# Performance work log

Hardware: AMD Instinct MI355X
Metric: run time of the kernel (lower is better)

Reference implementation:

```python
import jax, jax.numpy as jnp
import numpy as np

N, M, G, D = 64, 8, 64, 4
TAU_SPECIES = 5.0

def _psd(key, batch_shape):
    # random SPD matrices: 0.3*A A^T + 0.5 I
    A = 0.3 * jax.random.normal(key, (*batch_shape, D, D), dtype=jnp.float32)
    I = jnp.eye(D, dtype=jnp.float32)
    return jnp.einsum('...ij,...kj->...ik', A, A) + 0.5 * I

def _invertible(key, batch_shape):
    I = jnp.eye(D, dtype=jnp.float32)
    return I + 0.1 * jax.random.normal(key, (*batch_shape, D, D), dtype=jnp.float32)

def setup_inputs() -> dict:
    key = jax.random.key(0)
    ks = jax.random.split(key, 7)
    return {
        'mu_a': jax.random.normal(ks[0], (N, G, G, D), dtype=jnp.float32),
        'sigma_a': _psd(ks[1], (N, G, G)),
        'omega_a': _invertible(ks[2], (N, G, G)),
        'mu_b': jax.random.normal(ks[3], (M, G, G, D), dtype=jnp.float32),
        'sigma_b': _psd(ks[4], (M, G, G)),
        'omega_b': _invertible(ks[5], (M, G, G)),
        'chi': jax.random.uniform(ks[6], (N, G, G), dtype=jnp.float32),
    }

def reference(mu_a, sigma_a, omega_a, mu_b, sigma_b, omega_b, chi):
    # transport: Omega_a @ Omega_b^{-1}, pairwise over (N, M) and pointwise over grid
    omega_b_inv = jnp.linalg.inv(omega_b)                                  # (M,G,G,D,D)
    transport = jnp.einsum('nghij,mghjk->nmghik', omega_a, omega_b_inv)    # (N,M,G,G,D,D)
    mu_b_t = jnp.einsum('nmghij,mghj->nmghi', transport, mu_b)             # (N,M,G,G,D)
    sigma_b_t = jnp.einsum('nmghij,mghjk,nmghlk->nmghil',
                           transport, sigma_b, transport)                  # (N,M,G,G,D,D)
    # KL( N(mu_a, sigma_a) || N(mu_b_t, sigma_b_t) ), pointwise
    sig_b_inv = jnp.linalg.inv(sigma_b_t)
    diff = mu_a[:, None] - mu_b_t                                          # (N,M,G,G,D)
    tr = jnp.einsum('nmghij,nghji->nmgh', sig_b_inv, sigma_a)
    mahal = jnp.einsum('nmghi,nmghij,nmghj->nmgh', diff, sig_b_inv, diff)
    ld_b = jnp.linalg.slogdet(sigma_b_t)[1]                                # (N,M,G,G)
    ld_a = jnp.linalg.slogdet(sigma_a)[1]                                  # (N,G,G)
    kl = 0.5 * (tr + mahal - D + ld_b - ld_a[:, None])
    # species gate, masked by agent support chi_i(x)
    S = jax.nn.sigmoid(-kl / TAU_SPECIES) * chi[:, None]
    return S
```

## Files before the change

### kernel.cpp

```cpp
#include <hip/hip_runtime.h>
#include <math.h>


namespace {

constexpr int kN = 64;
constexpr int kM = 8;
constexpr int kG = 64;
constexpr int kGH = kG * kG;
constexpr int kMB = kM * kGH;
constexpr float kInvTau = 1.0f / 5.0f;

__device__ __forceinline__ void load16(const float* __restrict__ p, int idx,
                                       float* __restrict__ o) {
    const float4* p4 = reinterpret_cast<const float4*>(p);
#pragma unroll
    for (int k = 0; k < 4; ++k) {
        float4 v = p4[idx * 4 + k];
        o[4 * k + 0] = v.x;
        o[4 * k + 1] = v.y;
        o[4 * k + 2] = v.z;
        o[4 * k + 3] = v.w;
    }
}

__device__ __forceinline__ float det4(const float* __restrict__ m) {
    float s0 = m[0] * m[5] - m[1] * m[4];
    float s1 = m[0] * m[6] - m[2] * m[4];
    float s2 = m[0] * m[7] - m[3] * m[4];
    float s3 = m[1] * m[6] - m[2] * m[5];
    float s4 = m[1] * m[7] - m[3] * m[5];
    float s5 = m[2] * m[7] - m[3] * m[6];
    float c5 = m[10] * m[15] - m[11] * m[14];
    float c4 = m[9] * m[15] - m[11] * m[13];
    float c3 = m[9] * m[14] - m[10] * m[13];
    float c2 = m[8] * m[15] - m[11] * m[12];
    float c1 = m[8] * m[14] - m[10] * m[12];
    float c0 = m[8] * m[13] - m[9] * m[12];
    return s0 * c5 - s1 * c4 + s2 * c3 + s3 * c2 - s4 * c1 + s5 * c0;
}

__device__ __forceinline__ float inv4(const float* __restrict__ m,
                                      float* __restrict__ inv) {
    float s0 = m[0] * m[5] - m[1] * m[4];
    float s1 = m[0] * m[6] - m[2] * m[4];
    float s2 = m[0] * m[7] - m[3] * m[4];
    float s3 = m[1] * m[6] - m[2] * m[5];
    float s4 = m[1] * m[7] - m[3] * m[5];
    float s5 = m[2] * m[7] - m[3] * m[6];
    float c5 = m[10] * m[15] - m[11] * m[14];
    float c4 = m[9] * m[15] - m[11] * m[13];
    float c3 = m[9] * m[14] - m[10] * m[13];
    float c2 = m[8] * m[15] - m[11] * m[12];
    float c1 = m[8] * m[14] - m[10] * m[12];
    float c0 = m[8] * m[13] - m[9] * m[12];
    float det = s0 * c5 - s1 * c4 + s2 * c3 + s3 * c2 - s4 * c1 + s5 * c0;
    float r = __builtin_amdgcn_rcpf(det);
    inv[0]  = ( m[5]  * c5 - m[6]  * c4 + m[7]  * c3) * r;
    inv[1]  = (-m[1]  * c5 + m[2]  * c4 - m[3]  * c3) * r;
    inv[2]  = ( m[13] * s5 - m[14] * s4 + m[15] * s3) * r;
    inv[3]  = (-m[9]  * s5 + m[10] * s4 - m[11] * s3) * r;
    inv[4]  = (-m[4]  * c5 + m[6]  * c2 - m[7]  * c1) * r;
    inv[5]  = ( m[0]  * c5 - m[2]  * c2 + m[3]  * c1) * r;
    inv[6]  = (-m[12] * s5 + m[14] * s2 - m[15] * s1) * r;
    inv[7]  = ( m[8]  * s5 - m[10] * s2 + m[11] * s1) * r;
    inv[8]  = ( m[4]  * c4 - m[5]  * c2 + m[7]  * c0) * r;
    inv[9]  = (-m[0]  * c4 + m[1]  * c2 - m[3]  * c0) * r;
    inv[10] = ( m[12] * s4 - m[13] * s2 + m[15] * s0) * r;
    inv[11] = (-m[8]  * s4 + m[9]  * s2 - m[11] * s0) * r;
    inv[12] = (-m[4]  * c3 + m[5]  * c1 - m[6]  * c0) * r;
    inv[13] = ( m[0]  * c3 - m[1]  * c1 + m[2]  * c0) * r;
    inv[14] = (-m[12] * s3 + m[13] * s1 - m[14] * s0) * r;
    inv[15] = ( m[8]  * s3 - m[9]  * s1 + m[10] * s0) * r;
    return det;
}

__global__ __launch_bounds__(256) void precompute_b_kernel(
    const float* __restrict__ mu_b,
    const float* __restrict__ sigma_b,
    const float* __restrict__ omega_b,
    float4* __restrict__ ws)
{
    const int idx = blockIdx.x * blockDim.x + threadIdx.x;
    float Sb[16], Ob[16];
    load16(sigma_b, idx, Sb);
    load16(omega_b, idx, Ob);
    float SbI[16], ObI[16];
    const float detSb = inv4(Sb, SbI);
    const float detOb = inv4(Ob, ObI);
    const float4 mb4 = reinterpret_cast<const float4*>(mu_b)[idx];
    const float mb[4] = {mb4.x, mb4.y, mb4.z, mb4.w};

    float R[16];
#pragma unroll
    for (int i = 0; i < 4; ++i)
#pragma unroll
        for (int k = 0; k < 4; ++k)
            R[i * 4 + k] = SbI[i * 4 + 0] * Ob[0 * 4 + k]
                         + SbI[i * 4 + 1] * Ob[1 * 4 + k]
                         + SbI[i * 4 + 2] * Ob[2 * 4 + k]
                         + SbI[i * 4 + 3] * Ob[3 * 4 + k];
    float Qf[10];
    int pi = 0;
#pragma unroll
    for (int i = 0; i < 4; ++i)
#pragma unroll
        for (int k = 0; k < 4; ++k) {
            if (k < i) continue;
            float q = Ob[0 * 4 + i] * R[0 * 4 + k]
                    + Ob[1 * 4 + i] * R[1 * 4 + k]
                    + Ob[2 * 4 + i] * R[2 * 4 + k]
                    + Ob[3 * 4 + i] * R[3 * 4 + k];
            Qf[pi++] = (i == k) ? q : 2.0f * q;
        }
    float v[4];
#pragma unroll
    for (int i = 0; i < 4; ++i)
        v[i] = ObI[i * 4 + 0] * mb[0] + ObI[i * 4 + 1] * mb[1]
             + ObI[i * 4 + 2] * mb[2] + ObI[i * 4 + 3] * mb[3];

    const float lb = __logf(fabsf(detSb)) - 2.0f * __logf(fabsf(detOb));

    ws[0 * kMB + idx] = make_float4(Qf[0], Qf[1], Qf[2], Qf[3]);
    ws[1 * kMB + idx] = make_float4(Qf[4], Qf[5], Qf[6], Qf[7]);
    ws[2 * kMB + idx] = make_float4(Qf[8], Qf[9], lb, 0.0f);
    ws[3 * kMB + idx] = make_float4(v[0], v[1], v[2], v[3]);
}

__global__ __launch_bounds__(256) void species_kernel(
    const float* __restrict__ mu_a,
    const float* __restrict__ sigma_a,
    const float* __restrict__ omega_a,
    const float* __restrict__ chi,
    const float4* __restrict__ ws,
    float* __restrict__ out)
{
    const int t = blockIdx.x * blockDim.x + threadIdx.x;
    const int gh = t & (kGH - 1);
    const int n = t >> 12;

    float Sa[16], Oa[16], OaI[16];
    load16(sigma_a, t, Sa);
    load16(omega_a, t, Oa);
    const float detOa = inv4(Oa, OaI);
    const float detSa = det4(Sa);
    const float la = __logf(fabsf(detSa)) - 2.0f * __logf(fabsf(detOa));
    const float4 ma4 = reinterpret_cast<const float4*>(mu_a)[t];
    const float ma[4] = {ma4.x, ma4.y, ma4.z, ma4.w};
    const float x = chi[t];

    float w[4];
#pragma unroll
    for (int i = 0; i < 4; ++i)
        w[i] = OaI[i * 4 + 0] * ma[0] + OaI[i * 4 + 1] * ma[1]
             + OaI[i * 4 + 2] * ma[2] + OaI[i * 4 + 3] * ma[3];

    float Mt[16];
#pragma unroll
    for (int i = 0; i < 4; ++i)
#pragma unroll
        for (int k = 0; k < 4; ++k)
            Mt[i * 4 + k] = OaI[i * 4 + 0] * Sa[0 * 4 + k]
                          + OaI[i * 4 + 1] * Sa[1 * 4 + k]
                          + OaI[i * 4 + 2] * Sa[2 * 4 + k]
                          + OaI[i * 4 + 3] * Sa[3 * 4 + k];
    float Pf[10];
    {
        int pi = 0;
#pragma unroll
        for (int i = 0; i < 4; ++i)
#pragma unroll
            for (int k = 0; k < 4; ++k) {
                if (k < i) continue;
                Pf[pi++] = Mt[i * 4 + 0] * OaI[k * 4 + 0]
                         + Mt[i * 4 + 1] * OaI[k * 4 + 1]
                         + Mt[i * 4 + 2] * OaI[k * 4 + 2]
                         + Mt[i * 4 + 3] * OaI[k * 4 + 3];
            }
    }

#pragma unroll
    for (int m = 0; m < kM; ++m) {
        const int bb = m * kGH + gh;
        const float4 q0 = ws[0 * kMB + bb];
        const float4 q1 = ws[1 * kMB + bb];
        const float4 q2 = ws[2 * kMB + bb];
        const float4 q3 = ws[3 * kMB + bb];

        const float u0 = w[0] - q3.x;
        const float u1 = w[1] - q3.y;
        const float u2 = w[2] - q3.z;
        const float u3 = w[3] - q3.w;

        float tr = q0.x * Pf[0] + q0.y * Pf[1] + q0.z * Pf[2] + q0.w * Pf[3]
                 + q1.x * Pf[4] + q1.y * Pf[5] + q1.z * Pf[6] + q1.w * Pf[7]
                 + q2.x * Pf[8] + q2.y * Pf[9];
        float mah = q0.x * (u0 * u0) + q0.y * (u0 * u1) + q0.z * (u0 * u2)
                  + q0.w * (u0 * u3) + q1.x * (u1 * u1) + q1.y * (u1 * u2)
                  + q1.z * (u1 * u3) + q1.w * (u2 * u2) + q2.x * (u2 * u3)
                  + q2.y * (u3 * u3);

        const float kl = 0.5f * (tr + mah - 4.0f + q2.z - la);
        const float e = __expf(kl * kInvTau);
        const float s = x * __builtin_amdgcn_rcpf(1.0f + e);
        out[(n * kM + m) * kGH + gh] = s;
    }
}

}

extern "C" void kernel_launch(void* const* d_in, const int* in_sizes, int n_in,
                              void* d_out, int out_size, void* d_ws, size_t ws_size,
                              hipStream_t stream) {
    const float* mu_a    = (const float*)d_in[0];
    const float* sigma_a = (const float*)d_in[1];
    const float* omega_a = (const float*)d_in[2];
    const float* mu_b    = (const float*)d_in[3];
    const float* sigma_b = (const float*)d_in[4];
    const float* omega_b = (const float*)d_in[5];
    const float* chi     = (const float*)d_in[6];
    float* out = (float*)d_out;
    float4* ws = (float4*)d_ws;

    precompute_b_kernel<<<kMB / 256, 256, 0, stream>>>(mu_b, sigma_b, omega_b, ws);

    const int threads = kN * kGH;
    species_kernel<<<threads / 256, 256, 0, stream>>>(
        mu_a, sigma_a, omega_a, chi, ws, out);
}
```

Baseline: 98.22 us.

## Split species kernel across M with shared-memory staged coalesced A loads

Each block now handles 64 grid points, with four thread rows each computing two of the eight M outputs instead of one thread computing all eight. The sigma_a and omega_a matrices are loaded cooperatively with coalesced float4 reads into padded shared memory and then read back per thread. This raises thread-level parallelism and fixes the strided per-thread global loads. In exchange, every row redundantly recomputes the per-point A-side inverse and quadratic forms, adding a barrier and four times the A-side arithmetic.

```diff
diff --git a/kernel.cpp b/kernel.cpp
--- a/kernel.cpp
+++ b/kernel.cpp
@@ -10,6 +10,7 @@
 constexpr int kGH = kG * kG;
 constexpr int kMB = kM * kGH;
 constexpr float kInvTau = 1.0f / 5.0f;
+constexpr int kPad = 20;
 
 __device__ __forceinline__ void load16(const float* __restrict__ p, int idx,
                                        float* __restrict__ o) {
@@ -135,19 +136,41 @@
     const float4* __restrict__ ws,
     float* __restrict__ out)
 {
-    const int t = blockIdx.x * blockDim.x + threadIdx.x;
-    const int gh = t & (kGH - 1);
-    const int n = t >> 12;
+    __shared__ float sS[64 * kPad];
+    __shared__ float sO[64 * kPad];
+
+    const int x = threadIdx.x;
+    const int y = threadIdx.y;
+    const int tid = y * 64 + x;
+    const int t0 = blockIdx.x * 64;
+    const int t = t0 + x;
+    const int gh = (t0 & (kGH - 1)) + x;
+    const int n = t0 >> 12;
+
+    {
+        const float4* gs = reinterpret_cast<const float4*>(sigma_a) + (size_t)t0 * 4;
+        const float4* go = reinterpret_cast<const float4*>(omega_a) + (size_t)t0 * 4;
+        const float4 vs = gs[tid];
+        const float4 vo = go[tid];
+        const int xr = tid >> 2;
+        const int kk = (tid & 3) * 4;
+        *reinterpret_cast<float4*>(&sS[xr * kPad + kk]) = vs;
+        *reinterpret_cast<float4*>(&sO[xr * kPad + kk]) = vo;
+    }
+    __syncthreads();
 
     float Sa[16], Oa[16], OaI[16];
-    load16(sigma_a, t, Sa);
-    load16(omega_a, t, Oa);
+#pragma unroll
+    for (int j = 0; j < 16; ++j) {
+        Sa[j] = sS[x * kPad + j];
+        Oa[j] = sO[x * kPad + j];
+    }
     const float detOa = inv4(Oa, OaI);
     const float detSa = det4(Sa);
     const float la = __logf(fabsf(detSa)) - 2.0f * __logf(fabsf(detOa));
     const float4 ma4 = reinterpret_cast<const float4*>(mu_a)[t];
     const float ma[4] = {ma4.x, ma4.y, ma4.z, ma4.w};
-    const float x = chi[t];
+    const float xchi = chi[t];
 
     float w[4];
 #pragma unroll
@@ -180,7 +203,8 @@
     }
 
 #pragma unroll
-    for (int m = 0; m < kM; ++m) {
+    for (int h = 0; h < 2; ++h) {
+        const int m = y + 4 * h;
         const int bb = m * kGH + gh;
         const float4 q0 = ws[0 * kMB + bb];
         const float4 q1 = ws[1 * kMB + bb];
@@ -202,7 +226,7 @@
 
         const float kl = 0.5f * (tr + mah - 4.0f + q2.z - la);
         const float e = __expf(kl * kInvTau);
-        const float s = x * __builtin_amdgcn_rcpf(1.0f + e);
+        const float s = xchi * __builtin_amdgcn_rcpf(1.0f + e);
         out[(n * kM + m) * kGH + gh] = s;
     }
 }
@@ -224,7 +248,7 @@
 
     precompute_b_kernel<<<kMB / 256, 256, 0, stream>>>(mu_b, sigma_b, omega_b, ws);
 
-    const int threads = kN * kGH;
-    species_kernel<<<threads / 256, 256, 0, stream>>>(
+    dim3 block(64, 4);
+    species_kernel<<<kN * kGH / 64, block, 0, stream>>>(
         mu_a, sigma_a, omega_a, chi, ws, out);
 }
```

After: 99.67 us. About the same (+1.5%).

## Move per-A precompute into merged precompute kernel alongside B precompute

Applied to the files above, without the earlier changes.

Merges the B-side and A-side per-point precomputation into one kernel launch using block-index dispatch, writing A-side quadratic form terms, log-determinant, chi and transformed mean to workspace. The species kernel then only reads precomputed A and B factors and evaluates the pairwise KL gate. This aims to fill the GPU during the small B precompute and slim the main kernel, at the cost of extra workspace write and read traffic for the A terms.

```diff
diff --git a/kernel.cpp b/kernel.cpp
--- a/kernel.cpp
+++ b/kernel.cpp
@@ -9,6 +9,7 @@
 constexpr int kG = 64;
 constexpr int kGH = kG * kG;
 constexpr int kMB = kM * kGH;
+constexpr int kNA = kN * kGH;
 constexpr float kInvTau = 1.0f / 5.0f;
 
 __device__ __forceinline__ void load16(const float* __restrict__ p, int idx,
@@ -75,97 +76,90 @@
     return det;
 }
 
-__global__ __launch_bounds__(256) void precompute_b_kernel(
+__global__ __launch_bounds__(256) void precompute_kernel(
+    const float* __restrict__ mu_a,
+    const float* __restrict__ sigma_a,
+    const float* __restrict__ omega_a,
+    const float* __restrict__ chi,
     const float* __restrict__ mu_b,
     const float* __restrict__ sigma_b,
     const float* __restrict__ omega_b,
     float4* __restrict__ ws)
 {
-    const int idx = blockIdx.x * blockDim.x + threadIdx.x;
-    float Sb[16], Ob[16];
-    load16(sigma_b, idx, Sb);
-    load16(omega_b, idx, Ob);
-    float SbI[16], ObI[16];
-    const float detSb = inv4(Sb, SbI);
-    const float detOb = inv4(Ob, ObI);
-    const float4 mb4 = reinterpret_cast<const float4*>(mu_b)[idx];
-    const float mb[4] = {mb4.x, mb4.y, mb4.z, mb4.w};
-
-    float R[16];
-#pragma unroll
-    for (int i = 0; i < 4; ++i)
-#pragma unroll
-        for (int k = 0; k < 4; ++k)
-            R[i * 4 + k] = SbI[i * 4 + 0] * Ob[0 * 4 + k]
-                         + SbI[i * 4 + 1] * Ob[1 * 4 + k]
-                         + SbI[i * 4 + 2] * Ob[2 * 4 + k]
-                         + SbI[i * 4 + 3] * Ob[3 * 4 + k];
-    float Qf[10];
-    int pi = 0;
-#pragma unroll
-    for (int i = 0; i < 4; ++i)
-#pragma unroll
-        for (int k = 0; k < 4; ++k) {
-            if (k < i) continue;
-            float q = Ob[0 * 4 + i] * R[0 * 4 + k]
-                    + Ob[1 * 4 + i] * R[1 * 4 + k]
-                    + Ob[2 * 4 + i] * R[2 * 4 + k]
-                    + Ob[3 * 4 + i] * R[3 * 4 + k];
-            Qf[pi++] = (i == k) ? q : 2.0f * q;
-        }
-    float v[4];
-#pragma unroll
-    for (int i = 0; i < 4; ++i)
-        v[i] = ObI[i * 4 + 0] * mb[0] + ObI[i * 4 + 1] * mb[1]
-             + ObI[i * 4 + 2] * mb[2] + ObI[i * 4 + 3] * mb[3];
-
-    const float lb = __logf(fabsf(detSb)) - 2.0f * __logf(fabsf(detOb));
-
-    ws[0 * kMB + idx] = make_float4(Qf[0], Qf[1], Qf[2], Qf[3]);
-    ws[1 * kMB + idx] = make_float4(Qf[4], Qf[5], Qf[6], Qf[7]);
-    ws[2 * kMB + idx] = make_float4(Qf[8], Qf[9], lb, 0.0f);
-    ws[3 * kMB + idx] = make_float4(v[0], v[1], v[2], v[3]);
-}
-
-__global__ __launch_bounds__(256) void species_kernel(
-    const float* __restrict__ mu_a,
-    const float* __restrict__ sigma_a,
-    const float* __restrict__ omega_a,
-    const float* __restrict__ chi,
-    const float4* __restrict__ ws,
-    float* __restrict__ out)
-{
-    const int t = blockIdx.x * blockDim.x + threadIdx.x;
-    const int gh = t & (kGH - 1);
-    const int n = t >> 12;
-
-    float Sa[16], Oa[16], OaI[16];
-    load16(sigma_a, t, Sa);
-    load16(omega_a, t, Oa);
-    const float detOa = inv4(Oa, OaI);
-    const float detSa = det4(Sa);
-    const float la = __logf(fabsf(detSa)) - 2.0f * __logf(fabsf(detOa));
-    const float4 ma4 = reinterpret_cast<const float4*>(mu_a)[t];
-    const float ma[4] = {ma4.x, ma4.y, ma4.z, ma4.w};
-    const float x = chi[t];
-
-    float w[4];
-#pragma unroll
-    for (int i = 0; i < 4; ++i)
-        w[i] = OaI[i * 4 + 0] * ma[0] + OaI[i * 4 + 1] * ma[1]
-             + OaI[i * 4 + 2] * ma[2] + OaI[i * 4 + 3] * ma[3];
-
-    float Mt[16];
-#pragma unroll
-    for (int i = 0; i < 4; ++i)
-#pragma unroll
-        for (int k = 0; k < 4; ++k)
-            Mt[i * 4 + k] = OaI[i * 4 + 0] * Sa[0 * 4 + k]
-                          + OaI[i * 4 + 1] * Sa[1 * 4 + k]
-                          + OaI[i * 4 + 2] * Sa[2 * 4 + k]
-                          + OaI[i * 4 + 3] * Sa[3 * 4 + k];
-    float Pf[10];
-    {
+    const int blk = blockIdx.x;
+    if (blk < kMB / 256) {
+        const int idx = blk * 256 + threadIdx.x;
+        float Sb[16], Ob[16];
+        load16(sigma_b, idx, Sb);
+        load16(omega_b, idx, Ob);
+        float SbI[16], ObI[16];
+        const float detSb = inv4(Sb, SbI);
+        const float detOb = inv4(Ob, ObI);
+        const float4 mb4 = reinterpret_cast<const float4*>(mu_b)[idx];
+        const float mb[4] = {mb4.x, mb4.y, mb4.z, mb4.w};
+
+        float R[16];
+#pragma unroll
+        for (int i = 0; i < 4; ++i)
+#pragma unroll
+            for (int k = 0; k < 4; ++k)
+                R[i * 4 + k] = SbI[i * 4 + 0] * Ob[0 * 4 + k]
+                             + SbI[i * 4 + 1] * Ob[1 * 4 + k]
+                             + SbI[i * 4 + 2] * Ob[2 * 4 + k]
+                             + SbI[i * 4 + 3] * Ob[3 * 4 + k];
+        float Qf[10];
+        int pi = 0;
+#pragma unroll
+        for (int i = 0; i < 4; ++i)
+#pragma unroll
+            for (int k = 0; k < 4; ++k) {
+                if (k < i) continue;
+                float q = Ob[0 * 4 + i] * R[0 * 4 + k]
+                        + Ob[1 * 4 + i] * R[1 * 4 + k]
+                        + Ob[2 * 4 + i] * R[2 * 4 + k]
+                        + Ob[3 * 4 + i] * R[3 * 4 + k];
+                Qf[pi++] = (i == k) ? q : 2.0f * q;
+            }
+        float v[4];
+#pragma unroll
+        for (int i = 0; i < 4; ++i)
+            v[i] = ObI[i * 4 + 0] * mb[0] + ObI[i * 4 + 1] * mb[1]
+                 + ObI[i * 4 + 2] * mb[2] + ObI[i * 4 + 3] * mb[3];
+
+        const float lb = __logf(fabsf(detSb)) - 2.0f * __logf(fabsf(detOb));
+
+        ws[0 * kMB + idx] = make_float4(Qf[0], Qf[1], Qf[2], Qf[3]);
+        ws[1 * kMB + idx] = make_float4(Qf[4], Qf[5], Qf[6], Qf[7]);
+        ws[2 * kMB + idx] = make_float4(Qf[8], Qf[9], lb, 0.0f);
+        ws[3 * kMB + idx] = make_float4(v[0], v[1], v[2], v[3]);
+    } else {
+        const int t = (blk - kMB / 256) * 256 + threadIdx.x;
+        float Sa[16], Oa[16], OaI[16];
+        load16(sigma_a, t, Sa);
+        load16(omega_a, t, Oa);
+        const float detOa = inv4(Oa, OaI);
+        const float detSa = det4(Sa);
+        const float la = __logf(fabsf(detSa)) - 2.0f * __logf(fabsf(detOa));
+        const float4 ma4 = reinterpret_cast<const float4*>(mu_a)[t];
+        const float ma[4] = {ma4.x, ma4.y, ma4.z, ma4.w};
+        const float xchi = chi[t];
+
+        float w[4];
+#pragma unroll
+        for (int i = 0; i < 4; ++i)
+            w[i] = OaI[i * 4 + 0] * ma[0] + OaI[i * 4 + 1] * ma[1]
+                 + OaI[i * 4 + 2] * ma[2] + OaI[i * 4 + 3] * ma[3];
+
+        float Mt[16];
+#pragma unroll
+        for (int i = 0; i < 4; ++i)
+#pragma unroll
+            for (int k = 0; k < 4; ++k)
+                Mt[i * 4 + k] = OaI[i * 4 + 0] * Sa[0 * 4 + k]
+                              + OaI[i * 4 + 1] * Sa[1 * 4 + k]
+                              + OaI[i * 4 + 2] * Sa[2 * 4 + k]
+                              + OaI[i * 4 + 3] * Sa[3 * 4 + k];
+        float Pf[10];
         int pi = 0;
 #pragma unroll
         for (int i = 0; i < 4; ++i)
@@ -177,7 +171,30 @@
                          + Mt[i * 4 + 2] * OaI[k * 4 + 2]
                          + Mt[i * 4 + 3] * OaI[k * 4 + 3];
             }
+
+        float4* wsA = ws + 4 * kMB;
+        wsA[0 * kNA + t] = make_float4(Pf[0], Pf[1], Pf[2], Pf[3]);
+        wsA[1 * kNA + t] = make_float4(Pf[4], Pf[5], Pf[6], Pf[7]);
+        wsA[2 * kNA + t] = make_float4(Pf[8], Pf[9], la, xchi);
+        wsA[3 * kNA + t] = make_float4(w[0], w[1], w[2], w[3]);
     }
+}
+
+__global__ __launch_bounds__(256) void species_kernel(
+    const float4* __restrict__ ws,
+    float* __restrict__ out)
+{
+    const int t = blockIdx.x * blockDim.x + threadIdx.x;
+    const int gh = t & (kGH - 1);
+    const int n = t >> 12;
+
+    const float4* __restrict__ wsA = ws + 4 * kMB;
+    const float4 a0 = wsA[0 * kNA + t];
+    const float4 a1 = wsA[1 * kNA + t];
+    const float4 a2 = wsA[2 * kNA + t];
+    const float4 a3 = wsA[3 * kNA + t];
+    const float la = a2.z;
+    const float xchi = a2.w;
 
 #pragma unroll
     for (int m = 0; m < kM; ++m) {
@@ -187,14 +204,14 @@
         const float4 q2 = ws[2 * kMB + bb];
         const float4 q3 = ws[3 * kMB + bb];
 
-        const float u0 = w[0] - q3.x;
-        const float u1 = w[1] - q3.y;
-        const float u2 = w[2] - q3.z;
-        const float u3 = w[3] - q3.w;
-
-        float tr = q0.x * Pf[0] + q0.y * Pf[1] + q0.z * Pf[2] + q0.w * Pf[3]
-                 + q1.x * Pf[4] + q1.y * Pf[5] + q1.z * Pf[6] + q1.w * Pf[7]
-                 + q2.x * Pf[8] + q2.y * Pf[9];
+        const float u0 = a3.x - q3.x;
+        const float u1 = a3.y - q3.y;
+        const float u2 = a3.z - q3.z;
+        const float u3 = a3.w - q3.w;
+
+        float tr = q0.x * a0.x + q0.y * a0.y + q0.z * a0.z + q0.w * a0.w
+                 + q1.x * a1.x + q1.y * a1.y + q1.z * a1.z + q1.w * a1.w
+                 + q2.x * a2.x + q2.y * a2.y;
         float mah = q0.x * (u0 * u0) + q0.y * (u0 * u1) + q0.z * (u0 * u2)
                   + q0.w * (u0 * u3) + q1.x * (u1 * u1) + q1.y * (u1 * u2)
                   + q1.z * (u1 * u3) + q1.w * (u2 * u2) + q2.x * (u2 * u3)
@@ -202,7 +219,7 @@
 
         const float kl = 0.5f * (tr + mah - 4.0f + q2.z - la);
         const float e = __expf(kl * kInvTau);
-        const float s = x * __builtin_amdgcn_rcpf(1.0f + e);
+        const float s = xchi * __builtin_amdgcn_rcpf(1.0f + e);
         out[(n * kM + m) * kGH + gh] = s;
     }
 }
@@ -222,9 +239,10 @@
     float* out = (float*)d_out;
     float4* ws = (float4*)d_ws;
 
-    precompute_b_kernel<<<kMB / 256, 256, 0, stream>>>(mu_b, sigma_b, omega_b, ws);
-
-    const int threads = kN * kGH;
-    species_kernel<<<threads / 256, 256, 0, stream>>>(
-        mu_a, sigma_a, omega_a, chi, ws, out);
-}
+    const int nBlocksB = kMB / 256;
+    const int nBlocksA = kNA / 256;
+    precompute_kernel<<<nBlocksB + nBlocksA, 256, 0, stream>>>(
+        mu_a, sigma_a, omega_a, chi, mu_b, sigma_b, omega_b, ws);
+
+    species_kernel<<<kNA / 256, 256, 0, stream>>>(ws, out);
+}
```

After: 103.4 us. 1.05x slower.

## Split per-agent precompute and per-species evaluation across threads via shared memory

Applied to the files above, without the earlier changes.

Each block now handles 64 grid points. The first 64 threads compute the per-agent quantities (Pf, w, log-det, chi) and stage them in shared memory. After a barrier, all 512 threads evaluate one (point, species) pair each, where before one thread looped over all 8 species. This raises thread-level parallelism and memory-level parallelism for the ws loads and output stores. The cost is that 7/8 of threads sit idle during the precompute phase, plus a __syncthreads and an LDS round-trip.

```diff
diff --git a/kernel.cpp b/kernel.cpp
--- a/kernel.cpp
+++ b/kernel.cpp
@@ -9,6 +9,7 @@
 constexpr int kG = 64;
 constexpr int kGH = kG * kG;
 constexpr int kMB = kM * kGH;
+constexpr int kNA = kN * kGH;
 constexpr float kInvTau = 1.0f / 5.0f;
 
 __device__ __forceinline__ void load16(const float* __restrict__ p, int idx,
@@ -127,7 +128,7 @@
     ws[3 * kMB + idx] = make_float4(v[0], v[1], v[2], v[3]);
 }
 
-__global__ __launch_bounds__(256) void species_kernel(
+__global__ __launch_bounds__(512, 6) void species_kernel(
     const float* __restrict__ mu_a,
     const float* __restrict__ sigma_a,
     const float* __restrict__ omega_a,
@@ -135,37 +136,41 @@
     const float4* __restrict__ ws,
     float* __restrict__ out)
 {
-    const int t = blockIdx.x * blockDim.x + threadIdx.x;
-    const int gh = t & (kGH - 1);
-    const int n = t >> 12;
-
-    float Sa[16], Oa[16], OaI[16];
-    load16(sigma_a, t, Sa);
-    load16(omega_a, t, Oa);
-    const float detOa = inv4(Oa, OaI);
-    const float detSa = det4(Sa);
-    const float la = __logf(fabsf(detSa)) - 2.0f * __logf(fabsf(detOa));
-    const float4 ma4 = reinterpret_cast<const float4*>(mu_a)[t];
-    const float ma[4] = {ma4.x, ma4.y, ma4.z, ma4.w};
-    const float x = chi[t];
-
-    float w[4];
-#pragma unroll
-    for (int i = 0; i < 4; ++i)
-        w[i] = OaI[i * 4 + 0] * ma[0] + OaI[i * 4 + 1] * ma[1]
-             + OaI[i * 4 + 2] * ma[2] + OaI[i * 4 + 3] * ma[3];
-
-    float Mt[16];
-#pragma unroll
-    for (int i = 0; i < 4; ++i)
-#pragma unroll
-        for (int k = 0; k < 4; ++k)
-            Mt[i * 4 + k] = OaI[i * 4 + 0] * Sa[0 * 4 + k]
-                          + OaI[i * 4 + 1] * Sa[1 * 4 + k]
-                          + OaI[i * 4 + 2] * Sa[2 * 4 + k]
-                          + OaI[i * 4 + 3] * Sa[3 * 4 + k];
-    float Pf[10];
-    {
+    __shared__ float4 sAP[64 * 4];
+
+    const int tid = threadIdx.x;
+    const int t0 = blockIdx.x * 64;
+    const int gh0 = t0 & (kGH - 1);
+    const int n = t0 >> 12;
+
+    if (tid < 64) {
+        const int x = tid;
+        const int t = t0 + x;
+        float Sa[16], Oa[16], OaI[16];
+        load16(sigma_a, t, Sa);
+        load16(omega_a, t, Oa);
+        const float detOa = inv4(Oa, OaI);
+        const float detSa = det4(Sa);
+        const float la = __logf(fabsf(detSa)) - 2.0f * __logf(fabsf(detOa));
+        const float4 ma4 = reinterpret_cast<const float4*>(mu_a)[t];
+        const float xchi = chi[t];
+
+        float w[4];
+#pragma unroll
+        for (int i = 0; i < 4; ++i)
+            w[i] = OaI[i * 4 + 0] * ma4.x + OaI[i * 4 + 1] * ma4.y
+                 + OaI[i * 4 + 2] * ma4.z + OaI[i * 4 + 3] * ma4.w;
+
+        float Mt[16];
+#pragma unroll
+        for (int i = 0; i < 4; ++i)
+#pragma unroll
+            for (int k = 0; k < 4; ++k)
+                Mt[i * 4 + k] = OaI[i * 4 + 0] * Sa[0 * 4 + k]
+                              + OaI[i * 4 + 1] * Sa[1 * 4 + k]
+                              + OaI[i * 4 + 2] * Sa[2 * 4 + k]
+                              + OaI[i * 4 + 3] * Sa[3 * 4 + k];
+        float Pf[10];
         int pi = 0;
 #pragma unroll
         for (int i = 0; i < 4; ++i)
@@ -177,34 +182,46 @@
                          + Mt[i * 4 + 2] * OaI[k * 4 + 2]
                          + Mt[i * 4 + 3] * OaI[k * 4 + 3];
             }
+
+        sAP[x * 4 + 0] = make_float4(Pf[0], Pf[1], Pf[2], Pf[3]);
+        sAP[x * 4 + 1] = make_float4(Pf[4], Pf[5], Pf[6], Pf[7]);
+        sAP[x * 4 + 2] = make_float4(Pf[8], Pf[9], la, xchi);
+        sAP[x * 4 + 3] = make_float4(w[0], w[1], w[2], w[3]);
     }
-
-#pragma unroll
-    for (int m = 0; m < kM; ++m) {
-        const int bb = m * kGH + gh;
-        const float4 q0 = ws[0 * kMB + bb];
-        const float4 q1 = ws[1 * kMB + bb];
-        const float4 q2 = ws[2 * kMB + bb];
-        const float4 q3 = ws[3 * kMB + bb];
-
-        const float u0 = w[0] - q3.x;
-        const float u1 = w[1] - q3.y;
-        const float u2 = w[2] - q3.z;
-        const float u3 = w[3] - q3.w;
-
-        float tr = q0.x * Pf[0] + q0.y * Pf[1] + q0.z * Pf[2] + q0.w * Pf[3]
-                 + q1.x * Pf[4] + q1.y * Pf[5] + q1.z * Pf[6] + q1.w * Pf[7]
-                 + q2.x * Pf[8] + q2.y * Pf[9];
-        float mah = q0.x * (u0 * u0) + q0.y * (u0 * u1) + q0.z * (u0 * u2)
-                  + q0.w * (u0 * u3) + q1.x * (u1 * u1) + q1.y * (u1 * u2)
-                  + q1.z * (u1 * u3) + q1.w * (u2 * u2) + q2.x * (u2 * u3)
-                  + q2.y * (u3 * u3);
-
-        const float kl = 0.5f * (tr + mah - 4.0f + q2.z - la);
-        const float e = __expf(kl * kInvTau);
-        const float s = x * __builtin_amdgcn_rcpf(1.0f + e);
-        out[(n * kM + m) * kGH + gh] = s;
-    }
+    __syncthreads();
+
+    const int x = tid & 63;
+    const int m = tid >> 6;
+    const int gh = gh0 + x;
+
+    const float4 a0 = sAP[x * 4 + 0];
+    const float4 a1 = sAP[x * 4 + 1];
+    const float4 a2 = sAP[x * 4 + 2];
+    const float4 a3 = sAP[x * 4 + 3];
+
+    const int bb = m * kGH + gh;
+    const float4 q0 = ws[0 * kMB + bb];
+    const float4 q1 = ws[1 * kMB + bb];
+    const float4 q2 = ws[2 * kMB + bb];
+    const float4 q3 = ws[3 * kMB + bb];
+
+    const float u0 = a3.x - q3.x;
+    const float u1 = a3.y - q3.y;
+    const float u2 = a3.z - q3.z;
+    const float u3 = a3.w - q3.w;
+
+    float tr = q0.x * a0.x + q0.y * a0.y + q0.z * a0.z + q0.w * a0.w
+             + q1.x * a1.x + q1.y * a1.y + q1.z * a1.z + q1.w * a1.w
+             + q2.x * a2.x + q2.y * a2.y;
+    float mah = q0.x * (u0 * u0) + q0.y * (u0 * u1) + q0.z * (u0 * u2)
+              + q0.w * (u0 * u3) + q1.x * (u1 * u1) + q1.y * (u1 * u2)
+              + q1.z * (u1 * u3) + q1.w * (u2 * u2) + q2.x * (u2 * u3)
+              + q2.y * (u3 * u3);
+
+    const float kl = 0.5f * (tr + mah - 4.0f + q2.z - a2.z);
+    const float e = __expf(kl * kInvTau);
+    const float s = a2.w * __builtin_amdgcn_rcpf(1.0f + e);
+    out[(n * kM + m) * kGH + gh] = s;
 }
 
 }
@@ -224,7 +241,6 @@
 
     precompute_b_kernel<<<kMB / 256, 256, 0, stream>>>(mu_b, sigma_b, omega_b, ws);
 
-    const int threads = kN * kGH;
-    species_kernel<<<threads / 256, 256, 0, stream>>>(
+    species_kernel<<<kNA / 64, 512, 0, stream>>>(
         mu_a, sigma_a, omega_a, chi, ws, out);
 }
```

Result: slower. 103.4 us (+5.3%).
